# Kernel tuning notes

Measured on AMD Instinct MI355X. Metric: run time of the kernel, lower is better.

## Reference

```python
import jax, jax.numpy as jnp
import numpy as np


def _sage(x_src, x_dst, si, di, wl, b, wr):
    # out = x_dst @ wl^T + b  (self projection)
    out = x_dst @ wl.T + b
    n_dst = x_dst.shape[0]
    # mean aggregation of gathered source features over destination nodes
    agg = jax.ops.segment_sum(x_src[si], di, num_segments=n_dst)  # [N_dst, D]
    cnt = jax.ops.segment_sum(jnp.ones(si.shape, x_src.dtype), di, num_segments=n_dst)
    agg = agg / jnp.maximum(cnt, 1.0)[:, None]
    out = out + agg @ wr.T
    # F.normalize(p=2, dim=-1) with eps=1e-12
    norm = jnp.linalg.norm(out, axis=-1, keepdims=True)
    return out / jnp.maximum(norm, 1e-12)


def setup_inputs() -> dict:
    key = jax.random.key(0)
    ks = jax.random.split(key, 32)
    NA, NE, NF, D, E = 100000, 200000, 100000, 128, 400000
    inp = {
        'x_article': jax.random.normal(ks[0], (NA, D), jnp.float32),
        'x_entity': jax.random.normal(ks[1], (NE, D), jnp.float32),
        'x_fact': jax.random.normal(ks[2], (NF, D), jnp.float32),
    }
    # edge indices per EDGE_TYPES order
    srcs = [NA, NA, NE, NE, NF]
    dsts = [NE, NF, NA, NF, NE]
    for i in range(5):
        inp[f'si{i}'] = jax.random.randint(ks[3 + 2 * i], (E,), 0, srcs[i], jnp.int32)
        inp[f'di{i}'] = jax.random.randint(ks[4 + 2 * i], (E,), 0, dsts[i], jnp.int32)
    # per-edge-type params: W_l [out,in], b [out], W_r [out,in]
    scale = 1.0 / np.sqrt(D)
    for i in range(5):
        inp[f'wl{i}'] = jax.random.normal(ks[13 + 3 * i], (D, D), jnp.float32) * scale
        inp[f'b{i}'] = jnp.zeros((D,), jnp.float32)
        inp[f'wr{i}'] = jax.random.normal(ks[14 + 3 * i], (D, D), jnp.float32) * scale
    return inp


def reference(x_article, x_entity, x_fact,
              si0, di0, si1, di1, si2, di2, si3, di3, si4, di4,
              wl0, b0, wr0, wl1, b1, wr1, wl2, b2, wr2,
              wl3, b3, wr3, wl4, b4, wr4):
    # EDGE_TYPES: (article->entity), (article->fact), (entity->article),
    #             (entity->fact), (fact->entity); contributions to same dst are summed
    out_entity = _sage(x_article, x_entity, si0, di0, wl0, b0, wr0)
    out_fact = _sage(x_article, x_fact, si1, di1, wl1, b1, wr1)
    out_article = _sage(x_entity, x_article, si2, di2, wl2, b2, wr2)
    out_fact = out_fact + _sage(x_entity, x_fact, si3, di3, wl3, b3, wr3)
    out_entity = out_entity + _sage(x_fact, x_entity, si4, di4, wl4, b4, wr4)
    return out_article, out_entity, out_fact
```

## Files before the change

kernel.cpp:

```cpp
#include <hip/hip_runtime.h>
#include <hip/hip_bf16.h>

typedef __bf16 bf16;
typedef __attribute__((ext_vector_type(8))) __bf16 bf16x8;
typedef __attribute__((ext_vector_type(4))) float f32x4;

static __device__ inline bf16x8 pack_bf16x8(f32x4 lo, f32x4 hi) {
    bf16x8 t;
#pragma unroll
    for (int j = 0; j < 4; ++j) {
        t[j]     = (__bf16)lo[j];
        t[4 + j] = (__bf16)hi[j];
    }
    return t;
}

struct WConvArgs { const float* w[10]; bf16* dst; };

__global__ __launch_bounds__(256)
void convert_w(WConvArgs A) {
    int mat = blockIdx.y;
    int tid = blockIdx.x * 256 + threadIdx.x;
    if (tid >= 2048) return;
    int m  = tid & 15;
    int q  = (tid >> 4) & 3;
    int kc = (tid >> 6) & 3;
    int ct = tid >> 8;
    const float* src = A.w[mat] + (size_t)(ct * 16 + m) * 128 + kc * 32 + q * 8;
    bf16x8 t;
#pragma unroll
    for (int j = 0; j < 8; ++j) t[j] = (__bf16)src[j];
    bf16* dst = A.dst + (size_t)mat * 16384 + ((ct * 4 + kc) * 4 + q) * 128 + m * 8;
    *(bf16x8*)dst = t;
}

struct CsrArgs {
    const int* si[2];
    const int* di[2];
    int* ofs[2];
    int* tick[2];
    int* esrc[2];
    int* bsum[2];
    int E[2];
    int n1[2];
};

__global__ __launch_bounds__(256)
void csr_zero(CsrArgs A) {
    int t = blockIdx.y;
    int i = blockIdx.x * 256 + threadIdx.x;
    if (i < A.n1[t]) A.ofs[t][i] = 0;
}

__global__ __launch_bounds__(256)
void csr_hist(CsrArgs A) {
    int t = blockIdx.y;
    int E = A.E[t];
    const int* di = A.di[t];
    int* ofs = A.ofs[t];
    for (int i = blockIdx.x * 256 + threadIdx.x; i < E; i += gridDim.x * 256)
        atomicAdd(&ofs[di[i] + 1], 1);
}

__global__ __launch_bounds__(256)
void csr_scan_blocks(CsrArgs A) {
    __shared__ int lds[256];
    int ty = blockIdx.y;
    int n = A.n1[ty];
    int* a = A.ofs[ty];
    int* bsum = A.bsum[ty];
    int t = threadIdx.x;
    int base = blockIdx.x * 2048 + t * 8;
    int v[8];
    int run = 0;
#pragma unroll
    for (int j = 0; j < 8; ++j) {
        int idx = base + j;
        int x = (idx < n) ? a[idx] : 0;
        run += x;
        v[j] = run;
    }
    lds[t] = run;
    __syncthreads();
#pragma unroll
    for (int off = 1; off < 256; off <<= 1) {
        int x = (t >= off) ? lds[t - off] : 0;
        __syncthreads();
        lds[t] += x;
        __syncthreads();
    }
    int excl = t ? lds[t - 1] : 0;
#pragma unroll
    for (int j = 0; j < 8; ++j) {
        int idx = base + j;
        if (idx < n) a[idx] = v[j] + excl;
    }
    if (t == 255) bsum[blockIdx.x] = lds[255];
}

__global__ __launch_bounds__(256)
void csr_scan_bsums(CsrArgs A, int nb) {
    __shared__ int lds[256];
    int ty = blockIdx.x;
    int* bsum = A.bsum[ty];
    int t = threadIdx.x;
    int carry = 0;
    for (int base = 0; base < nb; base += 256) {
        int i = base + t;
        int v = (i < nb) ? bsum[i] : 0;
        lds[t] = v;
        __syncthreads();
#pragma unroll
        for (int off = 1; off < 256; off <<= 1) {
            int x = (t >= off) ? lds[t - off] : 0;
            __syncthreads();
            lds[t] += x;
            __syncthreads();
        }
        int excl = t ? lds[t - 1] : 0;
        if (i < nb) bsum[i] = excl + carry;
        carry += lds[255];
        __syncthreads();
    }
}

__global__ __launch_bounds__(256)
void csr_scan_add(CsrArgs A) {
    int ty = blockIdx.y;
    int n = A.n1[ty];
    int* a = A.ofs[ty];
    const int* bsum = A.bsum[ty];
    int* tick = A.tick[ty];
    int i = blockIdx.x * 256 + threadIdx.x;
    if (i < n) {
        int v = a[i] + bsum[i >> 11];
        a[i] = v;
        if (i < n - 1) tick[i] = v;
    }
}

__global__ __launch_bounds__(256)
void csr_fill(CsrArgs A) {
    int ty = blockIdx.y;
    int E = A.E[ty];
    const int* si = A.si[ty];
    const int* di = A.di[ty];
    int* tick = A.tick[ty];
    int* esrc = A.esrc[ty];
    for (int i = blockIdx.x * 256 + threadIdx.x; i < E; i += gridDim.x * 256) {
        int pos = atomicAdd(&tick[di[i]], 1);
        pos = pos < 0 ? 0 : (pos >= E ? E - 1 : pos);
        esrc[pos] = si[i];
    }
}

struct SageArgs {
    const float* xdst;
    float* out;
    int nd;
    int nc;
    const float* xsrc[2];
    const int* ofs[2];
    const int* esrc[2];
    const bf16* wf[2];
    const float* bias[2];
    int nsrc[2];
    int E[2];
};

__global__ __launch_bounds__(256)
void sage_fused(SageArgs A) {
    int lane = threadIdx.x & 63;
    int wave = threadIdx.x >> 6;
    int m = lane & 15;
    int q = lane >> 4;
    int nd = A.nd;
    int r0 = blockIdx.x * 64 + wave * 16;
    int rl = min(r0 + m, nd - 1);

    bf16x8 a1[4];
    const f32x4* xrow = (const f32x4*)(A.xdst + (size_t)rl * 128);
#pragma unroll
    for (int kc = 0; kc < 4; ++kc)
        a1[kc] = pack_bf16x8(xrow[kc * 8 + q * 2], xrow[kc * 8 + q * 2 + 1]);

    float ysum[8][4];
#pragma unroll
    for (int ct = 0; ct < 8; ++ct)
#pragma unroll
        for (int r = 0; r < 4; ++r) ysum[ct][r] = 0.f;

    for (int c = 0; c < A.nc; ++c) {
        const int* ofs  = A.ofs[c];
        const int* esrc = A.esrc[c];
        const float* xsrc = A.xsrc[c];
        int nsrc = A.nsrc[c];
        int Et   = A.E[c];

        int start = ofs[rl];
        int end   = ofs[rl + 1];
        start = start < 0 ? 0 : (start > Et ? Et : start);
        end   = end < start ? start : (end > Et ? Et : end);
        f32x4 aglo[4], aghi[4];
#pragma unroll
        for (int kc = 0; kc < 4; ++kc) {
            aglo[kc] = (f32x4){0.f, 0.f, 0.f, 0.f};
            aghi[kc] = (f32x4){0.f, 0.f, 0.f, 0.f};
        }
        int e = start;
        for (; e + 2 <= end; e += 2) {
            int s0 = esrc[e];
            int s1 = esrc[e + 1];
            s0 = s0 < 0 ? 0 : (s0 >= nsrc ? nsrc - 1 : s0);
            s1 = s1 < 0 ? 0 : (s1 >= nsrc ? nsrc - 1 : s1);
            const f32x4* p0 = (const f32x4*)(xsrc + (size_t)s0 * 128 + q * 8);
            const f32x4* p1 = (const f32x4*)(xsrc + (size_t)s1 * 128 + q * 8);
#pragma unroll
            for (int kc = 0; kc < 4; ++kc) {
                f32x4 u0 = p0[kc * 8], v0 = p0[kc * 8 + 1];
                f32x4 u1 = p1[kc * 8], v1 = p1[kc * 8 + 1];
                aglo[kc] += u0 + u1;
                aghi[kc] += v0 + v1;
            }
        }
        if (e < end) {
            int s0 = esrc[e];
            s0 = s0 < 0 ? 0 : (s0 >= nsrc ? nsrc - 1 : s0);
            const f32x4* p0 = (const f32x4*)(xsrc + (size_t)s0 * 128 + q * 8);
#pragma unroll
            for (int kc = 0; kc < 4; ++kc) {
                aglo[kc] += p0[kc * 8];
                aghi[kc] += p0[kc * 8 + 1];
            }
        }
        float invc = 1.0f / (float)max(end - start, 1);
        bf16x8 a2[4];
#pragma unroll
        for (int kc = 0; kc < 4; ++kc) {
            bf16x8 t;
#pragma unroll
            for (int j = 0; j < 4; ++j) {
                t[j]     = (__bf16)(aglo[kc][j] * invc);
                t[4 + j] = (__bf16)(aghi[kc][j] * invc);
            }
            a2[kc] = t;
        }

        const bf16x8* wf = (const bf16x8*)A.wf[c];
        int fb = q * 16 + m;
        f32x4 acc[8];
#pragma unroll
        for (int ct = 0; ct < 8; ++ct) {
            f32x4 cc = {0.f, 0.f, 0.f, 0.f};
#pragma unroll
            for (int kc = 0; kc < 4; ++kc) {
                bf16x8 bl = wf[(ct * 4 + kc) * 64 + fb];
                bf16x8 br = wf[2048 + (ct * 4 + kc) * 64 + fb];
                cc = __builtin_amdgcn_mfma_f32_16x16x32_bf16(a1[kc], bl, cc, 0, 0, 0);
                cc = __builtin_amdgcn_mfma_f32_16x16x32_bf16(a2[kc], br, cc, 0, 0, 0);
            }
            acc[ct] = cc;
        }

        const float* bias = A.bias[c];
        float ss[4] = {0.f, 0.f, 0.f, 0.f};
#pragma unroll
        for (int ct = 0; ct < 8; ++ct) {
            float bb = bias[ct * 16 + m];
#pragma unroll
            for (int r = 0; r < 4; ++r) {
                float v = acc[ct][r] + bb;
                acc[ct][r] = v;
                ss[r] += v * v;
            }
        }
#pragma unroll
        for (int off = 1; off < 16; off <<= 1) {
#pragma unroll
            for (int r = 0; r < 4; ++r) ss[r] += __shfl_xor(ss[r], off);
        }
        float sc[4];
#pragma unroll
        for (int r = 0; r < 4; ++r) sc[r] = 1.0f / fmaxf(sqrtf(ss[r]), 1e-12f);
#pragma unroll
        for (int ct = 0; ct < 8; ++ct)
#pragma unroll
            for (int r = 0; r < 4; ++r) ysum[ct][r] += acc[ct][r] * sc[r];
    }

#pragma unroll
    for (int r = 0; r < 4; ++r) {
        int orow = r0 + q * 4 + r;
        if (orow < nd) {
            float* op = A.out + (size_t)orow * 128 + m;
#pragma unroll
            for (int ct = 0; ct < 8; ++ct) op[ct * 16] = ysum[ct][r];
        }
    }
}

extern "C" void kernel_launch(void* const* d_in, const int* in_sizes, int n_in,
                              void* d_out, int out_size, void* d_ws, size_t ws_size,
                              hipStream_t stream) {
    const int D = 128;
    const float* x_article = (const float*)d_in[0];
    const float* x_entity  = (const float*)d_in[1];
    const float* x_fact    = (const float*)d_in[2];
    int NA = in_sizes[0] / D;
    int NE = in_sizes[1] / D;
    int NF = in_sizes[2] / D;

    const int* si[5];
    const int* di[5];
    for (int i = 0; i < 5; ++i) {
        si[i] = (const int*)d_in[3 + 2 * i];
        di[i] = (const int*)d_in[4 + 2 * i];
    }
    const float *wl[5], *bia[5], *wr[5];
    for (int i = 0; i < 5; ++i) {
        wl[i]  = (const float*)d_in[13 + 3 * i];
        bia[i] = (const float*)d_in[14 + 3 * i];
        wr[i]  = (const float*)d_in[15 + 3 * i];
    }

    float* outp = (float*)d_out;
    float* out_article = outp;
    float* out_entity  = outp + (size_t)NA * D;
    float* out_fact    = outp + (size_t)(NA + NE) * D;

    const float* xsrc[5] = {x_article, x_article, x_entity, x_entity, x_fact};
    int nsrcs[5] = {NA, NA, NE, NE, NF};

    bf16* wfrag = (bf16*)d_ws;
    WConvArgs wa;
    for (int t = 0; t < 5; ++t) {
        wa.w[t * 2]     = wl[t];
        wa.w[t * 2 + 1] = wr[t];
    }
    wa.dst = wfrag;
    convert_w<<<dim3(8, 10), 256, 0, stream>>>(wa);

    int* csr_base = (int*)((char*)d_ws + (size_t)5 * 32768 * sizeof(bf16));

    int grp_types[3][2] = {{2, -1}, {0, 4}, {1, 3}};
    int grp_nt[3] = {1, 2, 2};
    const float* grp_xdst[3] = {x_article, x_entity, x_fact};
    float* grp_out[3] = {out_article, out_entity, out_fact};
    int grp_nd[3] = {NA, NE, NF};

    for (int g = 0; g < 3; ++g) {
        int nt = grp_nt[g];
        int nd = grp_nd[g];
        int n1 = nd + 1;
        CsrArgs ca = {};
        SageArgs sa = {};
        int* p = csr_base;
        int Emax = 0;
        for (int k = 0; k < nt; ++k) {
            int t = grp_types[g][k];
            int E = in_sizes[3 + 2 * t];
            ca.si[k] = si[t];
            ca.di[k] = di[t];
            ca.ofs[k]  = p; p += n1;
            ca.tick[k] = p; p += nd;
            ca.esrc[k] = p; p += E;
            ca.bsum[k] = p; p += 256;
            ca.E[k] = E;
            ca.n1[k] = n1;
            if (E > Emax) Emax = E;
            sa.xsrc[k] = xsrc[t];
            sa.ofs[k]  = ca.ofs[k];
            sa.esrc[k] = ca.esrc[k];
            sa.wf[k]   = wfrag + (size_t)t * 32768;
            sa.bias[k] = bia[t];
            sa.nsrc[k] = nsrcs[t];
            sa.E[k]    = E;
        }
        int blk = (n1 + 255) / 256;
        int nb  = (n1 + 2047) / 2048;
        csr_zero<<<dim3(blk, nt), 256, 0, stream>>>(ca);
        csr_hist<<<dim3(1024, nt), 256, 0, stream>>>(ca);
        csr_scan_blocks<<<dim3(nb, nt), 256, 0, stream>>>(ca);
        csr_scan_bsums<<<dim3(nt), 256, 0, stream>>>(ca, nb);
        csr_scan_add<<<dim3(blk, nt), 256, 0, stream>>>(ca);
        csr_fill<<<dim3(1024, nt), 256, 0, stream>>>(ca);

        sa.xdst = grp_xdst[g];
        sa.out  = grp_out[g];
        sa.nd   = nd;
        sa.nc   = nt;
        sage_fused<<<(nd + 63) / 64, 256, 0, stream>>>(sa);
    }
}
```

Baseline: 979.5 us.

## Pre-convert node features to bf16 and batch all CSR builds and SAGE groups

```diff
diff --git a/kernel.cpp b/kernel.cpp
--- a/kernel.cpp
+++ b/kernel.cpp
@@ -34,15 +34,30 @@
     *(bf16x8*)dst = t;
 }
 
+struct XConvArgs { const float* src[3]; bf16* dst[3]; long long n8[3]; };
+
+__global__ __launch_bounds__(256)
+void convert_x(XConvArgs A) {
+    int a = blockIdx.y;
+    const float* s = A.src[a];
+    bf16* d = A.dst[a];
+    long long n8 = A.n8[a];
+    for (long long i = blockIdx.x * 256LL + threadIdx.x; i < n8;
+         i += (long long)gridDim.x * 256) {
+        const f32x4* p = (const f32x4*)(s + i * 8);
+        ((bf16x8*)d)[i] = pack_bf16x8(p[0], p[1]);
+    }
+}
+
 struct CsrArgs {
-    const int* si[2];
-    const int* di[2];
-    int* ofs[2];
-    int* tick[2];
-    int* esrc[2];
-    int* bsum[2];
-    int E[2];
-    int n1[2];
+    const int* si[5];
+    const int* di[5];
+    int* ofs[5];
+    int* tick[5];
+    int* esrc[5];
+    int* bsum[5];
+    int E[5];
+    int n1[5];
 };
 
 __global__ __launch_bounds__(256)
@@ -154,35 +169,48 @@
     }
 }
 
-struct SageArgs {
-    const float* xdst;
-    float* out;
-    int nd;
-    int nc;
-    const float* xsrc[2];
-    const int* ofs[2];
-    const int* esrc[2];
-    const bf16* wf[2];
-    const float* bias[2];
-    int nsrc[2];
-    int E[2];
+struct SageAll {
+    int bend[3];
+    int nd[3];
+    int nc[3];
+    const float* xdst_f[3];
+    const bf16*  xdst_b[3];
+    float* out[3];
+    const float* xsrc_f[3][2];
+    const bf16*  xsrc_b[3][2];
+    const int* ofs[3][2];
+    const int* esrc[3][2];
+    const bf16* wf[3][2];
+    const float* bias[3][2];
+    int nsrc[3][2];
+    int E[3][2];
 };
 
-__global__ __launch_bounds__(256)
-void sage_fused(SageArgs A) {
+template<int BF16S>
+__global__ __launch_bounds__(256)
+void sage_all(SageAll A) {
+    int bid = blockIdx.x;
+    int g = (bid >= A.bend[0]) + (bid >= A.bend[1]);
+    int bloc = bid - (g ? A.bend[g - 1] : 0);
     int lane = threadIdx.x & 63;
     int wave = threadIdx.x >> 6;
     int m = lane & 15;
     int q = lane >> 4;
-    int nd = A.nd;
-    int r0 = blockIdx.x * 64 + wave * 16;
+    int nd = A.nd[g];
+    int r0 = bloc * 64 + wave * 16;
     int rl = min(r0 + m, nd - 1);
 
     bf16x8 a1[4];
-    const f32x4* xrow = (const f32x4*)(A.xdst + (size_t)rl * 128);
-#pragma unroll
-    for (int kc = 0; kc < 4; ++kc)
-        a1[kc] = pack_bf16x8(xrow[kc * 8 + q * 2], xrow[kc * 8 + q * 2 + 1]);
+    if constexpr (BF16S) {
+        const bf16x8* xr = (const bf16x8*)(A.xdst_b[g] + (size_t)rl * 128);
+#pragma unroll
+        for (int kc = 0; kc < 4; ++kc) a1[kc] = xr[kc * 4 + q];
+    } else {
+        const f32x4* xrow = (const f32x4*)(A.xdst_f[g] + (size_t)rl * 128);
+#pragma unroll
+        for (int kc = 0; kc < 4; ++kc)
+            a1[kc] = pack_bf16x8(xrow[kc * 8 + q * 2], xrow[kc * 8 + q * 2 + 1]);
+    }
 
     float ysum[8][4];
 #pragma unroll
@@ -190,49 +218,85 @@
 #pragma unroll
         for (int r = 0; r < 4; ++r) ysum[ct][r] = 0.f;
 
-    for (int c = 0; c < A.nc; ++c) {
-        const int* ofs  = A.ofs[c];
-        const int* esrc = A.esrc[c];
-        const float* xsrc = A.xsrc[c];
-        int nsrc = A.nsrc[c];
-        int Et   = A.E[c];
+    int nc = A.nc[g];
+    for (int c = 0; c < nc; ++c) {
+        const int* ofs  = A.ofs[g][c];
+        const int* esrc = A.esrc[g][c];
+        int nsrc = A.nsrc[g][c];
+        int Et   = A.E[g][c];
 
         int start = ofs[rl];
         int end   = ofs[rl + 1];
         start = start < 0 ? 0 : (start > Et ? Et : start);
         end   = end < start ? start : (end > Et ? Et : end);
+
         f32x4 aglo[4], aghi[4];
 #pragma unroll
         for (int kc = 0; kc < 4; ++kc) {
             aglo[kc] = (f32x4){0.f, 0.f, 0.f, 0.f};
             aghi[kc] = (f32x4){0.f, 0.f, 0.f, 0.f};
         }
+
         int e = start;
-        for (; e + 2 <= end; e += 2) {
-            int s0 = esrc[e];
-            int s1 = esrc[e + 1];
-            s0 = s0 < 0 ? 0 : (s0 >= nsrc ? nsrc - 1 : s0);
-            s1 = s1 < 0 ? 0 : (s1 >= nsrc ? nsrc - 1 : s1);
-            const f32x4* p0 = (const f32x4*)(xsrc + (size_t)s0 * 128 + q * 8);
-            const f32x4* p1 = (const f32x4*)(xsrc + (size_t)s1 * 128 + q * 8);
-#pragma unroll
-            for (int kc = 0; kc < 4; ++kc) {
-                f32x4 u0 = p0[kc * 8], v0 = p0[kc * 8 + 1];
-                f32x4 u1 = p1[kc * 8], v1 = p1[kc * 8 + 1];
-                aglo[kc] += u0 + u1;
-                aghi[kc] += v0 + v1;
-            }
-        }
-        if (e < end) {
-            int s0 = esrc[e];
-            s0 = s0 < 0 ? 0 : (s0 >= nsrc ? nsrc - 1 : s0);
-            const f32x4* p0 = (const f32x4*)(xsrc + (size_t)s0 * 128 + q * 8);
-#pragma unroll
-            for (int kc = 0; kc < 4; ++kc) {
-                aglo[kc] += p0[kc * 8];
-                aghi[kc] += p0[kc * 8 + 1];
-            }
-        }
+        if constexpr (BF16S) {
+            const bf16* xs = A.xsrc_b[g][c];
+            for (; e + 2 <= end; e += 2) {
+                int s0 = esrc[e], s1 = esrc[e + 1];
+                s0 = s0 < 0 ? 0 : (s0 >= nsrc ? nsrc - 1 : s0);
+                s1 = s1 < 0 ? 0 : (s1 >= nsrc ? nsrc - 1 : s1);
+                const bf16x8* p0 = (const bf16x8*)(xs + (size_t)s0 * 128);
+                const bf16x8* p1 = (const bf16x8*)(xs + (size_t)s1 * 128);
+#pragma unroll
+                for (int kc = 0; kc < 4; ++kc) {
+                    bf16x8 v0 = p0[kc * 4 + q];
+                    bf16x8 v1 = p1[kc * 4 + q];
+#pragma unroll
+                    for (int j = 0; j < 4; ++j) {
+                        aglo[kc][j] += (float)v0[j] + (float)v1[j];
+                        aghi[kc][j] += (float)v0[4 + j] + (float)v1[4 + j];
+                    }
+                }
+            }
+            if (e < end) {
+                int s0 = esrc[e];
+                s0 = s0 < 0 ? 0 : (s0 >= nsrc ? nsrc - 1 : s0);
+                const bf16x8* p0 = (const bf16x8*)(xs + (size_t)s0 * 128);
+#pragma unroll
+                for (int kc = 0; kc < 4; ++kc) {
+                    bf16x8 v0 = p0[kc * 4 + q];
+#pragma unroll
+                    for (int j = 0; j < 4; ++j) {
+                        aglo[kc][j] += (float)v0[j];
+                        aghi[kc][j] += (float)v0[4 + j];
+                    }
+                }
+            }
+        } else {
+            const float* xs = A.xsrc_f[g][c];
+            for (; e + 2 <= end; e += 2) {
+                int s0 = esrc[e], s1 = esrc[e + 1];
+                s0 = s0 < 0 ? 0 : (s0 >= nsrc ? nsrc - 1 : s0);
+                s1 = s1 < 0 ? 0 : (s1 >= nsrc ? nsrc - 1 : s1);
+                const f32x4* p0 = (const f32x4*)(xs + (size_t)s0 * 128 + q * 8);
+                const f32x4* p1 = (const f32x4*)(xs + (size_t)s1 * 128 + q * 8);
+#pragma unroll
+                for (int kc = 0; kc < 4; ++kc) {
+                    aglo[kc] += p0[kc * 8] + p1[kc * 8];
+                    aghi[kc] += p0[kc * 8 + 1] + p1[kc * 8 + 1];
+                }
+            }
+            if (e < end) {
+                int s0 = esrc[e];
+                s0 = s0 < 0 ? 0 : (s0 >= nsrc ? nsrc - 1 : s0);
+                const f32x4* p0 = (const f32x4*)(xs + (size_t)s0 * 128 + q * 8);
+#pragma unroll
+                for (int kc = 0; kc < 4; ++kc) {
+                    aglo[kc] += p0[kc * 8];
+                    aghi[kc] += p0[kc * 8 + 1];
+                }
+            }
+        }
+
         float invc = 1.0f / (float)max(end - start, 1);
         bf16x8 a2[4];
 #pragma unroll
@@ -246,7 +310,7 @@
             a2[kc] = t;
         }
 
-        const bf16x8* wf = (const bf16x8*)A.wf[c];
+        const bf16x8* wf = (const bf16x8*)A.wf[g][c];
         int fb = q * 16 + m;
         f32x4 acc[8];
 #pragma unroll
@@ -262,7 +326,7 @@
             acc[ct] = cc;
         }
 
-        const float* bias = A.bias[c];
+        const float* bias = A.bias[g][c];
         float ss[4] = {0.f, 0.f, 0.f, 0.f};
 #pragma unroll
         for (int ct = 0; ct < 8; ++ct) {
@@ -292,7 +356,7 @@
     for (int r = 0; r < 4; ++r) {
         int orow = r0 + q * 4 + r;
         if (orow < nd) {
-            float* op = A.out + (size_t)orow * 128 + m;
+            float* op = A.out[g] + (size_t)orow * 128 + m;
 #pragma unroll
             for (int ct = 0; ct < 8; ++ct) op[ct * 16] = ysum[ct][r];
         }
@@ -303,18 +367,20 @@
                               void* d_out, int out_size, void* d_ws, size_t ws_size,
                               hipStream_t stream) {
     const int D = 128;
-    const float* x_article = (const float*)d_in[0];
-    const float* x_entity  = (const float*)d_in[1];
-    const float* x_fact    = (const float*)d_in[2];
+    const float* xarr[3] = {(const float*)d_in[0], (const float*)d_in[1],
+                            (const float*)d_in[2]};
     int NA = in_sizes[0] / D;
     int NE = in_sizes[1] / D;
     int NF = in_sizes[2] / D;
+    int nrow[3] = {NA, NE, NF};
 
     const int* si[5];
     const int* di[5];
+    int Et[5];
     for (int i = 0; i < 5; ++i) {
         si[i] = (const int*)d_in[3 + 2 * i];
         di[i] = (const int*)d_in[4 + 2 * i];
+        Et[i] = in_sizes[3 + 2 * i];
     }
     const float *wl[5], *bia[5], *wr[5];
     for (int i = 0; i < 5; ++i) {
@@ -324,12 +390,25 @@
     }
 
     float* outp = (float*)d_out;
-    float* out_article = outp;
-    float* out_entity  = outp + (size_t)NA * D;
-    float* out_fact    = outp + (size_t)(NA + NE) * D;
-
-    const float* xsrc[5] = {x_article, x_article, x_entity, x_entity, x_fact};
-    int nsrcs[5] = {NA, NA, NE, NE, NF};
+    float* grp_out[3] = {outp, outp + (size_t)NA * D, outp + (size_t)(NA + NE) * D};
+
+    int xsrc_idx[5] = {0, 0, 1, 1, 2};
+    int ndst[5]     = {NE, NF, NA, NF, NE};
+    int grp_types[3][2] = {{2, -1}, {0, 4}, {1, 3}};
+    int grp_nt[3]  = {1, 2, 2};
+    int grp_nd[3]  = {NA, NE, NF};
+    int grp_dst[3] = {0, 1, 2};
+
+    size_t wf_bytes = (size_t)5 * 32768 * sizeof(bf16);
+    size_t csr_all_ints = 0;
+    for (int t = 0; t < 5; ++t)
+        csr_all_ints += (size_t)(ndst[t] + 1) + ndst[t] + Et[t] + 128;
+    size_t xb_elems = ((size_t)NA + NE + NF) * D;
+
+    size_t off_csr = (wf_bytes + 15) & ~(size_t)15;
+    size_t off_xb  = (off_csr + csr_all_ints * 4 + 15) & ~(size_t)15;
+    int mode_full = (off_xb + xb_elems * sizeof(bf16)) <= ws_size;
+    int mode_lean = (off_csr + csr_all_ints * 4) <= ws_size;
 
     bf16* wfrag = (bf16*)d_ws;
     WConvArgs wa;
@@ -340,55 +419,93 @@
     wa.dst = wfrag;
     convert_w<<<dim3(8, 10), 256, 0, stream>>>(wa);
 
-    int* csr_base = (int*)((char*)d_ws + (size_t)5 * 32768 * sizeof(bf16));
-
-    int grp_types[3][2] = {{2, -1}, {0, 4}, {1, 3}};
-    int grp_nt[3] = {1, 2, 2};
-    const float* grp_xdst[3] = {x_article, x_entity, x_fact};
-    float* grp_out[3] = {out_article, out_entity, out_fact};
-    int grp_nd[3] = {NA, NE, NF};
-
-    for (int g = 0; g < 3; ++g) {
-        int nt = grp_nt[g];
-        int nd = grp_nd[g];
-        int n1 = nd + 1;
+    bf16* xb = (bf16*)((char*)d_ws + off_xb);
+    bf16* xb_arr[3] = {xb, xb + (size_t)NA * D, xb + ((size_t)NA + NE) * D};
+    if (mode_full) {
+        XConvArgs xa;
+        for (int a = 0; a < 3; ++a) {
+            xa.src[a] = xarr[a];
+            xa.dst[a] = xb_arr[a];
+            xa.n8[a]  = (long long)nrow[a] * 16;
+        }
+        convert_x<<<dim3(2048, 3), 256, 0, stream>>>(xa);
+    }
+
+    int* type_ofs[5];
+    int* type_esrc[5];
+    auto run_csr = [&](const int* types, int nt, int* base) {
         CsrArgs ca = {};
-        SageArgs sa = {};
-        int* p = csr_base;
-        int Emax = 0;
+        int* p = base;
+        int max_n1 = 0;
         for (int k = 0; k < nt; ++k) {
-            int t = grp_types[g][k];
-            int E = in_sizes[3 + 2 * t];
+            int t = types[k];
+            int nd = ndst[t], n1 = nd + 1, E = Et[t];
             ca.si[k] = si[t];
             ca.di[k] = di[t];
             ca.ofs[k]  = p; p += n1;
             ca.tick[k] = p; p += nd;
             ca.esrc[k] = p; p += E;
-            ca.bsum[k] = p; p += 256;
+            ca.bsum[k] = p; p += 128;
             ca.E[k] = E;
             ca.n1[k] = n1;
-            if (E > Emax) Emax = E;
-            sa.xsrc[k] = xsrc[t];
-            sa.ofs[k]  = ca.ofs[k];
-            sa.esrc[k] = ca.esrc[k];
-            sa.wf[k]   = wfrag + (size_t)t * 32768;
-            sa.bias[k] = bia[t];
-            sa.nsrc[k] = nsrcs[t];
-            sa.E[k]    = E;
-        }
-        int blk = (n1 + 255) / 256;
-        int nb  = (n1 + 2047) / 2048;
+            if (n1 > max_n1) max_n1 = n1;
+            type_ofs[t]  = ca.ofs[k];
+            type_esrc[t] = ca.esrc[k];
+        }
+        int blk = (max_n1 + 255) / 256;
+        int nb  = (max_n1 + 2047) / 2048;
         csr_zero<<<dim3(blk, nt), 256, 0, stream>>>(ca);
         csr_hist<<<dim3(1024, nt), 256, 0, stream>>>(ca);
         csr_scan_blocks<<<dim3(nb, nt), 256, 0, stream>>>(ca);
         csr_scan_bsums<<<dim3(nt), 256, 0, stream>>>(ca, nb);
         csr_scan_add<<<dim3(blk, nt), 256, 0, stream>>>(ca);
         csr_fill<<<dim3(1024, nt), 256, 0, stream>>>(ca);
-
-        sa.xdst = grp_xdst[g];
-        sa.out  = grp_out[g];
-        sa.nd   = nd;
-        sa.nc   = nt;
-        sage_fused<<<(nd + 63) / 64, 256, 0, stream>>>(sa);
-    }
-}
+    };
+
+    auto fill_group = [&](SageAll& sa, int slot, int g) {
+        sa.nd[slot] = grp_nd[g];
+        sa.nc[slot] = grp_nt[g];
+        sa.xdst_f[slot] = xarr[grp_dst[g]];
+        sa.xdst_b[slot] = xb_arr[grp_dst[g]];
+        sa.out[slot] = grp_out[g];
+        for (int c = 0; c < grp_nt[g]; ++c) {
+            int t = grp_types[g][c];
+            sa.xsrc_f[slot][c] = xarr[xsrc_idx[t]];
+            sa.xsrc_b[slot][c] = xb_arr[xsrc_idx[t]];
+            sa.ofs[slot][c]  = type_ofs[t];
+            sa.esrc[slot][c] = type_esrc[t];
+            sa.wf[slot][c]   = wfrag + (size_t)t * 32768;
+            sa.bias[slot][c] = bia[t];
+            sa.nsrc[slot][c] = nrow[xsrc_idx[t]];
+            sa.E[slot][c]    = Et[t];
+        }
+    };
+
+    int* csr_base = (int*)((char*)d_ws + off_csr);
+
+    if (mode_lean) {
+        int all_types[5] = {0, 1, 2, 3, 4};
+        run_csr(all_types, 5, csr_base);
+
+        SageAll sa = {};
+        int cum = 0;
+        for (int g = 0; g < 3; ++g) {
+            fill_group(sa, g, g);
+            cum += (grp_nd[g] + 63) / 64;
+            sa.bend[g] = cum;
+        }
+        if (mode_full)
+            sage_all<1><<<cum, 256, 0, stream>>>(sa);
+        else
+            sage_all<0><<<cum, 256, 0, stream>>>(sa);
+    } else {
+        for (int g = 0; g < 3; ++g) {
+            run_csr(grp_types[g], grp_nt[g], csr_base);
+            SageAll sa = {};
+            fill_group(sa, 0, g);
+            int nb = (grp_nd[g] + 63) / 64;
+            sa.bend[0] = nb; sa.bend[1] = nb; sa.bend[2] = nb;
+            sage_all<0><<<nb, 256, 0, stream>>>(sa);
+        }
+    }
+}
```

Result: no change. 982.1 us (+0.3%).
